# Performance work log

Hardware: AMD Instinct MI355X
Metric: run time of the kernel (lower is better)

## Reference

```python
import jax, jax.numpy as jnp
import numpy as np

EPS = 1e-6
NUM_HEADS = 16

def _rms(x, w=None):
    y = x * jax.lax.rsqrt(jnp.mean(x * x, axis=-1, keepdims=True) + EPS)
    return y if w is None else y * w

def _rope(q, k, pos):
    # q,k: [B,H,T,Dh]; half-split (rotate_half) RoPE convention, base 10000
    dh = q.shape[-1]
    half = dh // 2
    freqs = 1.0 / (10000.0 ** (jnp.arange(half, dtype=jnp.float32) / half))
    ang = pos.astype(jnp.float32)[:, None] * freqs[None, :]  # [T, half]
    cos = jnp.concatenate([jnp.cos(ang), jnp.cos(ang)], -1)  # [T, Dh]
    sin = jnp.concatenate([jnp.sin(ang), jnp.sin(ang)], -1)
    def rot(v):
        v1, v2 = jnp.split(v, 2, axis=-1)
        return jnp.concatenate([-v2, v1], -1)
    return q * cos + rot(q) * sin, k * cos + rot(k) * sin


def setup_inputs() -> dict:
    key = jax.random.key(0)
    ks = jax.random.split(key, 12)
    B, T, D, H = 2, 2048, 1024, NUM_HEADS
    Dh = D // H
    Hm = 2816  # SwiGLU hidden: multiple_of*ceil(int(2*4*D/3)/256)
    s = lambda fan_in: 1.0 / np.sqrt(fan_in)
    return {
        "x": jax.random.normal(ks[0], (B, T, D), jnp.float32),
        "c": jax.random.normal(ks[1], (B, D), jnp.float32),
        "pos": jnp.arange(T, dtype=jnp.int32),
        "adaln_w": jax.random.normal(ks[2], (D, 6 * D), jnp.float32) * s(D) * 0.1,
        "adaln_b": jax.random.normal(ks[3], (6 * D,), jnp.float32) * 0.02,
        "qkv_w": jax.random.normal(ks[4], (D, 3 * D), jnp.float32) * s(D),
        "lnq_w": jnp.ones((Dh,), jnp.float32),
        "lnk_w": jnp.ones((Dh,), jnp.float32),
        "proj_w": jax.random.normal(ks[5], (D, D), jnp.float32) * s(D),
        "proj_b": jnp.zeros((D,), jnp.float32),
        "w1_w": jax.random.normal(ks[6], (D, Hm), jnp.float32) * s(D),
        "w3_w": jax.random.normal(ks[7], (D, Hm), jnp.float32) * s(D),
        "w2_w": jax.random.normal(ks[8], (Hm, D), jnp.float32) * s(Hm),
    }


def reference(x, c, pos, adaln_w, adaln_b, qkv_w, lnq_w, lnk_w, proj_w, proj_b, w1_w, w3_w, w2_w):
    B, T, D = x.shape
    H = NUM_HEADS
    Dh = D // H

    # AdaLN: SiLU -> Linear -> chunk(6)
    mods = jax.nn.silu(c) @ adaln_w + adaln_b  # [B,6D]
    shift_msa, scale_msa, gate_msa, shift_mlp, scale_mlp, gate_mlp = jnp.split(mods, 6, axis=-1)

    # norm1 (RMSNorm, no affine) + modulate along seq dim
    x_mod = _rms(x) * (1.0 + scale_msa[:, None, :]) + shift_msa[:, None, :]

    # QKV projection (no bias)
    qkv = x_mod @ qkv_w  # [B,T,3D]
    q, k, v = jnp.split(qkv, 3, axis=-1)
    q = q.reshape(B, T, H, Dh).transpose(0, 2, 1, 3)  # [B,H,T,Dh]
    k = k.reshape(B, T, H, Dh).transpose(0, 2, 1, 3)
    v = v.reshape(B, T, H, Dh).transpose(0, 2, 1, 3)

    # per-head RMS qk-norm with affine weight
    q = _rms(q, lnq_w)
    k = _rms(k, lnk_w)

    # 1D RoPE
    q, k = _rope(q, k, pos)

    # attention core (SDPA, delegated in the original module)
    scores = jnp.einsum('bhqd,bhkd->bhqk', q, k) / jnp.sqrt(jnp.float32(Dh))
    attn = jax.nn.softmax(scores, axis=-1)
    attn_out = jnp.einsum('bhqk,bhkd->bhqd', attn, v)  # [B,H,T,Dh]
    attn_out = attn_out.transpose(0, 2, 1, 3).reshape(B, T, D)

    # post_attention: gated residual + SwiGLU MLP
    x = x + gate_msa[:, None, :] * (attn_out @ proj_w + proj_b)
    h = _rms(x) * (1.0 + scale_mlp[:, None, :]) + shift_mlp[:, None, :]
    mlp = (jax.nn.silu(h @ w1_w) * (h @ w3_w)) @ w2_w
    x = x + gate_mlp[:, None, :] * mlp
    return x
```

## Files before the change

### kernel.cpp

```cpp
#include <hip/hip_runtime.h>
#include <stdint.h>
#include <math.h>

typedef unsigned short u16;
typedef __attribute__((ext_vector_type(4))) float f32x4;
typedef __attribute__((ext_vector_type(16))) float f32x16;
typedef __attribute__((ext_vector_type(8))) __bf16 bf16x8;

#define DEV static __device__ __forceinline__

typedef __attribute__((address_space(1))) void gvoid;
typedef __attribute__((address_space(3))) void lvoid;

DEV float bf2f(u16 u){ uint32_t v = ((uint32_t)u) << 16; float f; __builtin_memcpy(&f, &v, 4); return f; }
DEV u16 f2bf(float f){ uint32_t v; __builtin_memcpy(&v, &f, 4); v = (v + 0x7fffu + ((v >> 16) & 1u)) >> 16; return (u16)v; }

DEV void cp16(const void* g, void* l){
  __builtin_amdgcn_global_load_lds((gvoid*)g, (lvoid*)l, 16, 0, 0);
}
DEV f32x4 mfma16(bf16x8 a, bf16x8 b, f32x4 c){
  return __builtin_amdgcn_mfma_f32_16x16x32_bf16(a, b, c, 0, 0, 0);
}
DEV f32x16 mfma32(bf16x8 a, bf16x8 b, f32x16 c){
  return __builtin_amdgcn_mfma_f32_32x32x16_bf16(a, b, c, 0, 0, 0);
}
DEV uint32_t cvtpk(float a, float b){
  uint32_t r;
  asm volatile("v_cvt_pk_bf16_f32 %0, %1, %2" : "=v"(r) : "v"(a), "v"(b));
  return r;
}
DEV void uswap(uint32_t& a, uint32_t& b){
  asm volatile("v_permlane32_swap_b32 %0, %1" : "+v"(a), "+v"(b));
}
DEV void fswap(float& a, float& b){
  asm volatile("v_permlane32_swap_b32 %0, %1" : "+v"(a), "+v"(b));
}
DEV float fexp2(float x){
  float r;
  asm("v_exp_f32 %0, %1" : "=v"(r) : "v"(x));
  return r;
}

DEV void slab_remap(int SX, int SY, int& bx, int& by)
{
  const int GX = gridDim.x;
  const int h = blockIdx.y * GX + blockIdx.x;
  const int x = h & 7, s = h >> 3;
  const int ssz = SX * SY;
  const int nsx = GX / SX;
  const int slab = x + 8 * (s / ssz);
  const int ws = s % ssz;
  bx = (slab % nsx) * SX + ws % SX;
  by = (slab / nsx) * SY + ws / SX;
}

__global__ void __launch_bounds__(256) adaln1(const float* __restrict__ c,
                                              const float* __restrict__ w,
                                              float* __restrict__ part)
{
  __shared__ float sc[256];
  int k0 = blockIdx.y * 128;
  {
    int i = threadIdx.x;
    int b = i >> 7, kk = i & 127;
    float v = c[b * 1024 + k0 + kk];
    sc[i] = v / (1.f + __expf(-v));
  }
  __syncthreads();
  int col = blockIdx.x * 256 + threadIdx.x;
  float a0 = 0.f, a1 = 0.f;
  #pragma unroll 8
  for (int k = 0; k < 128; ++k){
    float wv = w[(size_t)(k0 + k) * 6144 + col];
    a0 += sc[k] * wv;
    a1 += sc[128 + k] * wv;
  }
  part[((size_t)blockIdx.y * 2 + 0) * 6144 + col] = a0;
  part[((size_t)blockIdx.y * 2 + 1) * 6144 + col] = a1;
}

__global__ void __launch_bounds__(256) adaln2(const float* __restrict__ part,
                                              const float* __restrict__ bias,
                                              float* __restrict__ mods)
{
  int i = blockIdx.x * 256 + threadIdx.x;
  int b = i / 6144, col = i % 6144;
  float a = bias[col];
  #pragma unroll
  for (int r = 0; r < 8; ++r) a += part[((size_t)r * 2 + b) * 6144 + col];
  mods[i] = a;
}

__global__ void __launch_bounds__(256) rope_table(const int* __restrict__ pos,
                                                  float* __restrict__ ct,
                                                  float* __restrict__ st)
{
  int idx = blockIdx.x * 256 + threadIdx.x;
  int t = idx >> 5, i = idx & 31;
  float freq = expf(-0.28782313662425575f * (float)i);
  float ang = (float)pos[t] * freq;
  ct[idx] = cosf(ang);
  st[idx] = sinf(ang);
}

__global__ void __launch_bounds__(256) rmsmod(const float* __restrict__ x,
                                              const float* __restrict__ mods,
                                              u16* __restrict__ out,
                                              int shift_off, int scale_off)
{
  __shared__ float wsum[4];
  int row = blockIdx.x;
  int b = row >> 11;
  const float4 v = ((const float4*)(x + (size_t)row * 1024))[threadIdx.x];
  float ss = v.x * v.x + v.y * v.y + v.z * v.z + v.w * v.w;
  #pragma unroll
  for (int m = 1; m < 64; m <<= 1) ss += __shfl_xor(ss, m);
  if ((threadIdx.x & 63) == 0) wsum[threadIdx.x >> 6] = ss;
  __syncthreads();
  float tot = wsum[0] + wsum[1] + wsum[2] + wsum[3];
  float rr = rsqrtf(tot * (1.f / 1024.f) + 1e-6f);
  const float* mb = mods + (size_t)b * 6144;
  int d0 = threadIdx.x * 4;
  ushort4 o;
  o.x = f2bf(v.x * rr * (1.f + mb[scale_off + d0 + 0]) + mb[shift_off + d0 + 0]);
  o.y = f2bf(v.y * rr * (1.f + mb[scale_off + d0 + 1]) + mb[shift_off + d0 + 1]);
  o.z = f2bf(v.z * rr * (1.f + mb[scale_off + d0 + 2]) + mb[shift_off + d0 + 2]);
  o.w = f2bf(v.w * rr * (1.f + mb[scale_off + d0 + 3]) + mb[shift_off + d0 + 3]);
  ((ushort4*)(out + (size_t)row * 1024))[threadIdx.x] = o;
}

__global__ void __launch_bounds__(256) transpose_w(const float* __restrict__ in,
                                                   u16* __restrict__ out, int R, int C)
{
  __shared__ float t[32][33];
  int tx = threadIdx.x & 31, ty = threadIdx.x >> 5;
  int c0 = blockIdx.x * 32, r0 = blockIdx.y * 32;
  #pragma unroll
  for (int i = 0; i < 4; ++i) t[ty + 8 * i][tx] = in[(size_t)(r0 + ty + 8 * i) * C + c0 + tx];
  __syncthreads();
  #pragma unroll
  for (int i = 0; i < 4; ++i) out[(size_t)(c0 + ty + 8 * i) * R + r0 + tx] = f2bf(t[tx][ty + 8 * i]);
}

__global__ void __launch_bounds__(256) vtrans(const u16* __restrict__ qkv,
                                              u16* __restrict__ vt)
{
  __shared__ u16 tile[32][33];
  int tx = threadIdx.x & 31, ty = threadIdx.x >> 5;
  int t0 = blockIdx.x * 32;
  int d0 = blockIdx.y * 32;
  int bh = blockIdx.z; int b = bh >> 4, h = bh & 15;
  #pragma unroll
  for (int i = 0; i < 4; ++i) {
    int t = t0 + ty + 8 * i;
    tile[ty + 8 * i][tx] = qkv[((size_t)(b * 2048 + t)) * 3072 + 2048 + h * 64 + d0 + tx];
  }
  __syncthreads();
  #pragma unroll
  for (int i = 0; i < 4; ++i) {
    int d = d0 + ty + 8 * i;
    vt[((size_t)bh * 64 + d) * 2048 + t0 + tx] = tile[tx][ty + 8 * i];
  }
}

__global__ void __launch_bounds__(256) gemm_bt(const u16* __restrict__ A,
                                               const u16* __restrict__ Bt,
                                               int M, int N, int K,
                                               int SX, int SY,
                                               u16* __restrict__ outb)
{
  __shared__ __align__(16) u16 Ash[2][128 * 64];
  __shared__ __align__(16) u16 Bsh[2][128 * 64];
  const int tid = threadIdx.x;
  const int l = tid & 63, w = tid >> 6;
  int bx, by; slab_remap(SX, SY, bx, by);
  const int m0 = by * 128, n0 = bx * 128;
  const int wr = (w >> 1) * 64, wc = (w & 1) * 64;
  const int fr = l & 15, fg = l >> 4;
  const int sw = fr & 7;
  const int nk = K >> 6;
  f32x4 acc[4][4] = {};

  auto stage = [&](int kt, int bsel) {
    #pragma unroll
    for (int p = 0; p < 4; ++p) {
      int slot = p * 256 + tid;
      int r = slot >> 3, kp = slot & 7;
      int kpg = kp ^ (r & 7);
      cp16(A + (size_t)(m0 + r) * K + kt + kpg * 8, &Ash[bsel][slot * 8]);
      cp16(Bt + (size_t)(n0 + r) * K + kt + kpg * 8, &Bsh[bsel][slot * 8]);
    }
  };

  stage(0, 0);
  __syncthreads();

  for (int t = 0; t < nk; ++t) {
    if (t + 1 < nk) stage((t + 1) << 6, (t + 1) & 1);
    const u16* Ab = Ash[t & 1];
    const u16* Bb = Bsh[t & 1];
    #pragma unroll
    for (int kk = 0; kk < 2; ++kk) {
      const int coff = ((kk * 4 + fg) ^ sw) * 8;
      bf16x8 af[4], bfr[4];
      #pragma unroll
      for (int m = 0; m < 4; ++m) af[m] = *(const bf16x8*)(Ab + (wr + m * 16 + fr) * 64 + coff);
      #pragma unroll
      for (int n = 0; n < 4; ++n) bfr[n] = *(const bf16x8*)(Bb + (wc + n * 16 + fr) * 64 + coff);
      #pragma unroll
      for (int m = 0; m < 4; ++m)
        #pragma unroll
        for (int n = 0; n < 4; ++n)
          acc[m][n] = mfma16(af[m], bfr[n], acc[m][n]);
    }
    __syncthreads();
  }

  #pragma unroll
  for (int m = 0; m < 4; ++m)
  #pragma unroll
  for (int n = 0; n < 4; ++n)
  #pragma unroll
  for (int j = 0; j < 4; ++j) {
    int row = m0 + wr + m * 16 + fg * 4 + j;
    int col = n0 + wc + n * 16 + fr;
    outb[(size_t)row * N + col] = f2bf(acc[m][n][j]);
  }
}

template<int EPI>
__global__ void __launch_bounds__(256) gemm_skinny(const u16* __restrict__ A,
                                                   const u16* __restrict__ Bt,
                                                   int M, int N, int K,
                                                   const float* __restrict__ mods,
                                                   int gate_off,
                                                   const float* __restrict__ bias,
                                                   const float* __restrict__ res,
                                                   float* __restrict__ outf)
{
  __shared__ __align__(16) u16 Ash[2][64 * 64];
  __shared__ __align__(16) u16 Bsh[2][128 * 64];
  const int tid = threadIdx.x;
  const int l = tid & 63, w = tid >> 6;
  int bx, by; slab_remap(2, 16, bx, by);
  const int m0 = by * 64, n0 = bx * 128;
  const int wr = (w >> 1) * 32, wc = (w & 1) * 64;
  const int fr = l & 15, fg = l >> 4;
  const int sw = fr & 7;
  const int nk = K >> 6;
  f32x4 acc[2][4] = {};

  auto stage = [&](int kt, int bsel) {
    #pragma unroll
    for (int p = 0; p < 2; ++p) {
      int slot = p * 256 + tid;
      int r = slot >> 3, kp = slot & 7;
      int kpg = kp ^ (r & 7);
      cp16(A + (size_t)(m0 + r) * K + kt + kpg * 8, &Ash[bsel][slot * 8]);
    }
    #pragma unroll
    for (int p = 0; p < 4; ++p) {
      int slot = p * 256 + tid;
      int r = slot >> 3, kp = slot & 7;
      int kpg = kp ^ (r & 7);
      cp16(Bt + (size_t)(n0 + r) * K + kt + kpg * 8, &Bsh[bsel][slot * 8]);
    }
  };

  stage(0, 0);
  __syncthreads();

  for (int t = 0; t < nk; ++t) {
    if (t + 1 < nk) stage((t + 1) << 6, (t + 1) & 1);
    const u16* Ab = Ash[t & 1];
    const u16* Bb = Bsh[t & 1];
    #pragma unroll
    for (int kk = 0; kk < 2; ++kk) {
      const int coff = ((kk * 4 + fg) ^ sw) * 8;
      bf16x8 af[2], bfr[4];
      #pragma unroll
      for (int m = 0; m < 2; ++m) af[m] = *(const bf16x8*)(Ab + (wr + m * 16 + fr) * 64 + coff);
      #pragma unroll
      for (int n = 0; n < 4; ++n) bfr[n] = *(const bf16x8*)(Bb + (wc + n * 16 + fr) * 64 + coff);
      #pragma unroll
      for (int m = 0; m < 2; ++m)
        #pragma unroll
        for (int n = 0; n < 4; ++n)
          acc[m][n] = mfma16(af[m], bfr[n], acc[m][n]);
    }
    __syncthreads();
  }

  #pragma unroll
  for (int m = 0; m < 2; ++m)
  #pragma unroll
  for (int n = 0; n < 4; ++n)
  #pragma unroll
  for (int j = 0; j < 4; ++j) {
    int row = m0 + wr + m * 16 + fg * 4 + j;
    int col = n0 + wc + n * 16 + fr;
    size_t idx = (size_t)row * N + col;
    float v = acc[m][n][j];
    int b = row >> 11;
    if (EPI == 1)
      outf[idx] = res[idx] + mods[(size_t)b * 6144 + gate_off + col] * (v + bias[col]);
    else
      outf[idx] = res[idx] + mods[(size_t)b * 6144 + gate_off + col] * v;
  }
}

__global__ void __launch_bounds__(256) gemm_w13(const u16* __restrict__ A,
                                                const u16* __restrict__ B1t,
                                                const u16* __restrict__ B3t,
                                                u16* __restrict__ outb)
{
  const int K = 1024, N = 2816;
  __shared__ __align__(16) u16 Ash[2][128 * 64];
  __shared__ __align__(16) u16 B1sh[2][64 * 64];
  __shared__ __align__(16) u16 B3sh[2][64 * 64];
  const int tid = threadIdx.x;
  const int l = tid & 63, w = tid >> 6;
  int bx, by; slab_remap(11, 8, bx, by);
  const int m0 = by * 128, n0 = bx * 64;
  const int wr = (w >> 1) * 64, wc = (w & 1) * 32;
  const int fr = l & 15, fg = l >> 4;
  const int sw = fr & 7;
  f32x4 acc1[4][2] = {}, acc3[4][2] = {};

  auto stage = [&](int kt, int bsel) {
    #pragma unroll
    for (int p = 0; p < 4; ++p) {
      int slot = p * 256 + tid;
      int r = slot >> 3, kp = slot & 7;
      int kpg = kp ^ (r & 7);
      cp16(A + (size_t)(m0 + r) * K + kt + kpg * 8, &Ash[bsel][slot * 8]);
    }
    #pragma unroll
    for (int p = 0; p < 2; ++p) {
      int slot = p * 256 + tid;
      int r = slot >> 3, kp = slot & 7;
      int kpg = kp ^ (r & 7);
      cp16(B1t + (size_t)(n0 + r) * K + kt + kpg * 8, &B1sh[bsel][slot * 8]);
      cp16(B3t + (size_t)(n0 + r) * K + kt + kpg * 8, &B3sh[bsel][slot * 8]);
    }
  };

  stage(0, 0);
  __syncthreads();

  for (int t = 0; t < 16; ++t) {
    if (t + 1 < 16) stage((t + 1) << 6, (t + 1) & 1);
    const u16* Ab  = Ash[t & 1];
    const u16* B1b = B1sh[t & 1];
    const u16* B3b = B3sh[t & 1];
    #pragma unroll
    for (int kk = 0; kk < 2; ++kk) {
      const int coff = ((kk * 4 + fg) ^ sw) * 8;
      bf16x8 af[4], b1f[2], b3f[2];
      #pragma unroll
      for (int m = 0; m < 4; ++m) af[m] = *(const bf16x8*)(Ab + (wr + m * 16 + fr) * 64 + coff);
      #pragma unroll
      for (int n = 0; n < 2; ++n) {
        b1f[n] = *(const bf16x8*)(B1b + (wc + n * 16 + fr) * 64 + coff);
        b3f[n] = *(const bf16x8*)(B3b + (wc + n * 16 + fr) * 64 + coff);
      }
      #pragma unroll
      for (int m = 0; m < 4; ++m)
        #pragma unroll
        for (int n = 0; n < 2; ++n) {
          acc1[m][n] = mfma16(af[m], b1f[n], acc1[m][n]);
          acc3[m][n] = mfma16(af[m], b3f[n], acc3[m][n]);
        }
    }
    __syncthreads();
  }

  #pragma unroll
  for (int m = 0; m < 4; ++m)
  #pragma unroll
  for (int n = 0; n < 2; ++n)
  #pragma unroll
  for (int j = 0; j < 4; ++j) {
    int row = m0 + wr + m * 16 + fg * 4 + j;
    int col = n0 + wc + n * 16 + fr;
    float v1 = acc1[m][n][j];
    float v3 = acc3[m][n][j];
    float s = v1 / (1.f + __expf(-v1));
    outb[(size_t)row * N + col] = f2bf(s * v3);
  }
}

__global__ void __launch_bounds__(256) qknorm_rope(const u16* __restrict__ qkv,
                                                   const float* __restrict__ lnq,
                                                   const float* __restrict__ lnk,
                                                   const float* __restrict__ ctab,
                                                   const float* __restrict__ stab,
                                                   u16* __restrict__ qo,
                                                   u16* __restrict__ ko)
{
  int r = blockIdx.x * 4 + (threadIdx.x >> 6);
  int l = threadIdx.x & 63;
  int h = r & 15, t = (r >> 4) & 2047, b = r >> 15;
  const u16* base = qkv + ((size_t)(b * 2048 + t)) * 3072 + h * 64 + l;
  float q = bf2f(base[0]);
  float k = bf2f(base[1024]);
  float sq = q * q, sk = k * k;
  #pragma unroll
  for (int m = 1; m < 64; m <<= 1) { sq += __shfl_xor(sq, m); sk += __shfl_xor(sk, m); }
  float rq = rsqrtf(sq * (1.f / 64.f) + 1e-6f);
  float rk = rsqrtf(sk * (1.f / 64.f) + 1e-6f);
  float yq = q * rq * lnq[l];
  float yk = k * rk * lnk[l];
  float cs = ctab[t * 32 + (l & 31)];
  float sn = stab[t * 32 + (l & 31)];
  float pq = __shfl_xor(yq, 32);
  float pk = __shfl_xor(yk, 32);
  float rotq = (l < 32) ? -pq : pq;
  float rotk = (l < 32) ? -pk : pk;
  float oq = (yq * cs + rotq * sn) * 0.1803368801111204f;
  float ok = yk * cs + rotk * sn;
  size_t oidx = ((size_t)(b * 16 + h) * 2048 + t) * 64 + l;
  qo[oidx] = f2bf(oq);
  ko[oidx] = f2bf(ok);
}

__global__ void __launch_bounds__(256, 2) flash_attn(const u16* __restrict__ qg,
                                                     const u16* __restrict__ kg,
                                                     const u16* __restrict__ vtg,
                                                     u16* __restrict__ og)
{
  __shared__ __align__(16) char smem[65536];
  const int tid = threadIdx.x, l = tid & 63, w = tid >> 6;
  const int lq = l & 31, hi = l >> 5;
  const int swz = lq & 7;
  const int xcd = blockIdx.x & 7, slot = blockIdx.x >> 3;
  const int g = slot >> 4, qt = slot & 15;
  const int bh = g * 8 + xcd;
  const int h = bh & 15, b = bh >> 4;

  bf16x8 qf[4];
  {
    const u16* qp = qg + ((size_t)bh * 2048 + qt * 128 + w * 32 + lq) * 64 + hi * 8;
    #pragma unroll
    for (int ks = 0; ks < 4; ++ks) qf[ks] = *(const bf16x8*)(qp + ks * 16);
  }
  const u16* kgb = kg + (size_t)bh * 2048 * 64;
  const u16* vgb = vtg + (size_t)bh * 64 * 2048;

  auto stage = [&](int kv, int bsel) {
    #pragma unroll
    for (int p = 0; p < 4; ++p) {
      int s2 = p * 256 + tid;
      int r = s2 >> 3, cl = s2 & 7;
      int cg = cl ^ (r & 7);
      cp16(kgb + (size_t)(kv + r) * 64 + cg * 8, smem + bsel * 16384 + s2 * 16);
    }
    #pragma unroll
    for (int p = 0; p < 4; ++p) {
      int s2 = p * 256 + tid;
      int r = s2 >> 4, cl = s2 & 15;
      int cg = cl ^ (r & 7);
      cp16(vgb + (size_t)r * 2048 + kv + cg * 8, smem + 32768 + bsel * 16384 + s2 * 16);
    }
  };

  f32x16 ob0 = {}, ob1 = {};
  float l_run = 0.f;

  stage(0, 0);
  __syncthreads();

  for (int t = 0; t < 16; ++t) {
    const int cur = t & 1;
    stage(((t + 1) & 15) * 128, cur ^ 1);
    const char* Kb = smem + cur * 16384;
    const char* Vb = smem + 32768 + cur * 16384;

    #pragma unroll
    for (int ko = 0; ko < 128; ko += 64) {
      f32x16 s0 = {}, s1 = {};
      __builtin_amdgcn_s_setprio(1);
      #pragma unroll
      for (int ks = 0; ks < 4; ++ks) {
        const int c = hi + ks * 2;
        bf16x8 kf0 = *(const bf16x8*)(Kb + (ko + lq) * 128 + ((c ^ swz) << 4));
        bf16x8 kf1 = *(const bf16x8*)(Kb + (ko + 32 + lq) * 128 + ((c ^ swz) << 4));
        s0 = mfma32(kf0, qf[ks], s0);
        s1 = mfma32(kf1, qf[ks], s1);
      }
      __builtin_amdgcn_s_setprio(0);
      #pragma unroll
      for (int r = 0; r < 16; ++r) s0[r] = fexp2(s0[r]);
      #pragma unroll
      for (int r = 0; r < 16; ++r) s1[r] = fexp2(s1[r]);
      {
        float t0 = (s0[0] + s0[1]) + (s0[2] + s0[3]);
        float t1 = (s0[4] + s0[5]) + (s0[6] + s0[7]);
        float t2 = (s0[8] + s0[9]) + (s0[10] + s0[11]);
        float t3 = (s0[12] + s0[13]) + (s0[14] + s0[15]);
        float u0 = (s1[0] + s1[1]) + (s1[2] + s1[3]);
        float u1 = (s1[4] + s1[5]) + (s1[6] + s1[7]);
        float u2 = (s1[8] + s1[9]) + (s1[10] + s1[11]);
        float u3 = (s1[12] + s1[13]) + (s1[14] + s1[15]);
        float ls = ((t0 + t1) + (t2 + t3)) + ((u0 + u1) + (u2 + u3));
        float lo = ls;
        fswap(ls, lo);
        l_run += ls + lo;
      }
      uint32_t pw[16];
      {
        uint32_t x0 = cvtpk(s0[0], s0[1]),   y0 = cvtpk(s0[4], s0[5]);   uswap(x0, y0);
        uint32_t x1 = cvtpk(s0[2], s0[3]),   y1 = cvtpk(s0[6], s0[7]);   uswap(x1, y1);
        uint32_t x2 = cvtpk(s0[8], s0[9]),   y2 = cvtpk(s0[12], s0[13]); uswap(x2, y2);
        uint32_t x3 = cvtpk(s0[10], s0[11]), y3 = cvtpk(s0[14], s0[15]); uswap(x3, y3);
        pw[0] = x0; pw[1] = x1; pw[2] = y0; pw[3] = y1;
        pw[4] = x2; pw[5] = x3; pw[6] = y2; pw[7] = y3;
      }
      {
        uint32_t x0 = cvtpk(s1[0], s1[1]),   y0 = cvtpk(s1[4], s1[5]);   uswap(x0, y0);
        uint32_t x1 = cvtpk(s1[2], s1[3]),   y1 = cvtpk(s1[6], s1[7]);   uswap(x1, y1);
        uint32_t x2 = cvtpk(s1[8], s1[9]),   y2 = cvtpk(s1[12], s1[13]); uswap(x2, y2);
        uint32_t x3 = cvtpk(s1[10], s1[11]), y3 = cvtpk(s1[14], s1[15]); uswap(x3, y3);
        pw[8] = x0;  pw[9] = x1;  pw[10] = y0; pw[11] = y1;
        pw[12] = x2; pw[13] = x3; pw[14] = y2; pw[15] = y3;
      }
      __builtin_amdgcn_s_setprio(1);
      #pragma unroll
      for (int ks = 0; ks < 4; ++ks) {
        union { uint32_t u[4]; bf16x8 v; } pk_;
        pk_.u[0] = pw[ks * 4 + 0]; pk_.u[1] = pw[ks * 4 + 1];
        pk_.u[2] = pw[ks * 4 + 2]; pk_.u[3] = pw[ks * 4 + 3];
        const int c = (ko >> 3) + ks * 2 + hi;
        bf16x8 vf0 = *(const bf16x8*)(Vb + lq * 256 + ((c ^ swz) << 4));
        bf16x8 vf1 = *(const bf16x8*)(Vb + (32 + lq) * 256 + ((c ^ swz) << 4));
        ob0 = mfma32(vf0, pk_.v, ob0);
        ob1 = mfma32(vf1, pk_.v, ob1);
      }
      __builtin_amdgcn_s_setprio(0);
    }
    __syncthreads();
  }

  float invl = 1.0f / l_run;
  char* ob_base = smem + w * 4096 + lq * 128 + 8 * hi;
  #pragma unroll
  for (int g2 = 0; g2 < 4; ++g2) {
    uint2 t2;
    t2.x = cvtpk(ob0[g2 * 4 + 0] * invl, ob0[g2 * 4 + 1] * invl);
    t2.y = cvtpk(ob0[g2 * 4 + 2] * invl, ob0[g2 * 4 + 3] * invl);
    *(uint2*)(ob_base + ((g2 ^ (lq & 7)) << 4)) = t2;
    uint2 t3;
    t3.x = cvtpk(ob1[g2 * 4 + 0] * invl, ob1[g2 * 4 + 1] * invl);
    t3.y = cvtpk(ob1[g2 * 4 + 2] * invl, ob1[g2 * 4 + 3] * invl);
    *(uint2*)(ob_base + (((g2 + 4) ^ (lq & 7)) << 4)) = t3;
  }
  __syncthreads();
  #pragma unroll
  for (int i = 0; i < 4; ++i) {
    int idx = i * 256 + tid;
    int ww = idx >> 8, q = (idx >> 3) & 31, s = idx & 7;
    uint4 val = *(const uint4*)(smem + ww * 4096 + q * 128 + ((s ^ (q & 7)) << 4));
    int t = qt * 128 + ww * 32 + q;
    *(uint4*)(og + ((size_t)(b * 2048 + t)) * 1024 + h * 64 + s * 8) = val;
  }
}

extern "C" void kernel_launch(void* const* d_in, const int* in_sizes, int n_in,
                              void* d_out, int out_size, void* d_ws, size_t ws_size,
                              hipStream_t stream)
{
  (void)in_sizes; (void)n_in; (void)out_size; (void)ws_size;
  const float* x       = (const float*)d_in[0];
  const float* c       = (const float*)d_in[1];
  const int*   pos     = (const int*)d_in[2];
  const float* adaln_w = (const float*)d_in[3];
  const float* adaln_b = (const float*)d_in[4];
  const float* qkv_w   = (const float*)d_in[5];
  const float* lnq     = (const float*)d_in[6];
  const float* lnk     = (const float*)d_in[7];
  const float* proj_w  = (const float*)d_in[8];
  const float* proj_b  = (const float*)d_in[9];
  const float* w1_w    = (const float*)d_in[10];
  const float* w3_w    = (const float*)d_in[11];
  const float* w2_w    = (const float*)d_in[12];
  float* out = (float*)d_out;

  char* ws = (char*)d_ws;
  size_t off = 0;
  auto alloc = [&](size_t bytes) -> char* {
    char* p = ws + off; off += (bytes + 255) & ~(size_t)255; return p;
  };
  float* part    = (float*)alloc((size_t)8 * 2 * 6144 * 4);
  float* mods    = (float*)alloc((size_t)2 * 6144 * 4);
  float* ctab    = (float*)alloc((size_t)2048 * 32 * 4);
  float* stab    = (float*)alloc((size_t)2048 * 32 * 4);
  u16* qkv_wt    = (u16*)alloc((size_t)3072 * 1024 * 2);
  u16* proj_wt   = (u16*)alloc((size_t)1024 * 1024 * 2);
  u16* w1_wt     = (u16*)alloc((size_t)2816 * 1024 * 2);
  u16* w3_wt     = (u16*)alloc((size_t)2816 * 1024 * 2);
  u16* w2_wt     = (u16*)alloc((size_t)1024 * 2816 * 2);
  float* x1      = (float*)alloc((size_t)4096 * 1024 * 4);
  u16* attn_bf   = (u16*)alloc((size_t)4096 * 1024 * 2);
  char* pool = ws + off;
  u16* xmod_bf   = (u16*)(pool);
  u16* qkv_bf    = (u16*)(pool + 8388608);
  u16* q_bf      = (u16*)(pool + 33554432);
  u16* k_bf      = (u16*)(pool + 41943040);
  u16* vt_bf     = (u16*)(pool + 50331648);
  u16* h_bf      = (u16*)(pool);
  u16* hidden_bf = (u16*)(pool + 31457280);

  adaln1<<<dim3(24, 8), 256, 0, stream>>>(c, adaln_w, part);
  adaln2<<<48, 256, 0, stream>>>(part, adaln_b, mods);
  rope_table<<<256, 256, 0, stream>>>(pos, ctab, stab);
  rmsmod<<<4096, 256, 0, stream>>>(x, mods, xmod_bf, 0, 1024);
  transpose_w<<<dim3(96, 32), 256, 0, stream>>>(qkv_w, qkv_wt, 1024, 3072);
  transpose_w<<<dim3(32, 32), 256, 0, stream>>>(proj_w, proj_wt, 1024, 1024);
  transpose_w<<<dim3(88, 32), 256, 0, stream>>>(w1_w, w1_wt, 1024, 2816);
  transpose_w<<<dim3(88, 32), 256, 0, stream>>>(w3_w, w3_wt, 1024, 2816);
  transpose_w<<<dim3(32, 88), 256, 0, stream>>>(w2_w, w2_wt, 2816, 1024);

  gemm_bt<<<dim3(24, 32), 256, 0, stream>>>(xmod_bf, qkv_wt, 4096, 3072, 1024, 6, 8, qkv_bf);
  qknorm_rope<<<16384, 256, 0, stream>>>(qkv_bf, lnq, lnk, ctab, stab, q_bf, k_bf);
  vtrans<<<dim3(64, 2, 32), 256, 0, stream>>>(qkv_bf, vt_bf);
  flash_attn<<<512, 256, 0, stream>>>(q_bf, k_bf, vt_bf, attn_bf);
  gemm_skinny<1><<<dim3(8, 64), 256, 0, stream>>>(attn_bf, proj_wt, 4096, 1024, 1024,
                                                  mods, 2048, proj_b, x, x1);
  rmsmod<<<4096, 256, 0, stream>>>(x1, mods, h_bf, 3072, 4096);
  gemm_w13<<<dim3(44, 32), 256, 0, stream>>>(h_bf, w1_wt, w3_wt, hidden_bf);
  gemm_skinny<4><<<dim3(8, 64), 256, 0, stream>>>(hidden_bf, w2_wt, 4096, 1024, 2816,
                                                  mods, 5120, nullptr, x1, out);
}
```

Before: 270.4 us.

## Replace double-buffered K=64 staging with single-buffered K=32 tiles in QKV and W13 GEMMs

Drops the double-buffered 64-wide K staging (with an async prefetch of the next tile) from gemm_bt and gemm_w13. In its place is a single-buffered 32-wide K loop that syncs, loads, syncs and computes, with a simpler 4-way XOR swizzle. This cuts LDS usage a lot, which may allow more blocks per CU, but global-load latency is no longer overlapped with MFMA work and barriers per K element double. The slab_remap group size for w13 also changes from 8 to 4.

```diff
diff --git a/kernel.cpp b/kernel.cpp
--- a/kernel.cpp
+++ b/kernel.cpp
@@ -169,51 +169,43 @@
                                                int SX, int SY,
                                                u16* __restrict__ outb)
 {
-  __shared__ __align__(16) u16 Ash[2][128 * 64];
-  __shared__ __align__(16) u16 Bsh[2][128 * 64];
+  __shared__ __align__(16) u16 Ash[128 * 32];
+  __shared__ __align__(16) u16 Bsh[128 * 32];
   const int tid = threadIdx.x;
   const int l = tid & 63, w = tid >> 6;
   int bx, by; slab_remap(SX, SY, bx, by);
   const int m0 = by * 128, n0 = bx * 128;
   const int wr = (w >> 1) * 64, wc = (w & 1) * 64;
   const int fr = l & 15, fg = l >> 4;
-  const int sw = fr & 7;
-  const int nk = K >> 6;
   f32x4 acc[4][4] = {};
 
-  auto stage = [&](int kt, int bsel) {
-    #pragma unroll
-    for (int p = 0; p < 4; ++p) {
+  for (int kt = 0; kt < K; kt += 32) {
+    __syncthreads();
+    #pragma unroll
+    for (int p = 0; p < 2; ++p) {
       int slot = p * 256 + tid;
-      int r = slot >> 3, kp = slot & 7;
-      int kpg = kp ^ (r & 7);
-      cp16(A + (size_t)(m0 + r) * K + kt + kpg * 8, &Ash[bsel][slot * 8]);
-      cp16(Bt + (size_t)(n0 + r) * K + kt + kpg * 8, &Bsh[bsel][slot * 8]);
-    }
-  };
-
-  stage(0, 0);
-  __syncthreads();
-
-  for (int t = 0; t < nk; ++t) {
-    if (t + 1 < nk) stage((t + 1) << 6, (t + 1) & 1);
-    const u16* Ab = Ash[t & 1];
-    const u16* Bb = Bsh[t & 1];
-    #pragma unroll
-    for (int kk = 0; kk < 2; ++kk) {
-      const int coff = ((kk * 4 + fg) ^ sw) * 8;
-      bf16x8 af[4], bfr[4];
-      #pragma unroll
-      for (int m = 0; m < 4; ++m) af[m] = *(const bf16x8*)(Ab + (wr + m * 16 + fr) * 64 + coff);
-      #pragma unroll
-      for (int n = 0; n < 4; ++n) bfr[n] = *(const bf16x8*)(Bb + (wc + n * 16 + fr) * 64 + coff);
-      #pragma unroll
-      for (int m = 0; m < 4; ++m)
-        #pragma unroll
-        for (int n = 0; n < 4; ++n)
-          acc[m][n] = mfma16(af[m], bfr[n], acc[m][n]);
+      int r = slot >> 2, kp = slot & 3;
+      int kpg = kp ^ (r & 3);
+      cp16(A + (size_t)(m0 + r) * K + kt + kpg * 8, Ash + slot * 8);
+      cp16(Bt + (size_t)(n0 + r) * K + kt + kpg * 8, Bsh + slot * 8);
     }
     __syncthreads();
+    bf16x8 af[4], bfr[4];
+    #pragma unroll
+    for (int m = 0; m < 4; ++m) {
+      int r = wr + m * 16 + fr;
+      af[m] = *(const bf16x8*)(Ash + r * 32 + ((fg ^ (r & 3)) << 3));
+    }
+    #pragma unroll
+    for (int n = 0; n < 4; ++n) {
+      int r = wc + n * 16 + fr;
+      bfr[n] = *(const bf16x8*)(Bsh + r * 32 + ((fg ^ (r & 3)) << 3));
+    }
+    #pragma unroll
+    for (int m = 0; m < 4; ++m)
+      #pragma unroll
+      for (int n = 0; n < 4; ++n)
+        acc[m][n] = mfma16(af[m], bfr[n], acc[m][n]);
   }
 
   #pragma unroll
@@ -315,64 +307,53 @@
                                                 u16* __restrict__ outb)
 {
   const int K = 1024, N = 2816;
-  __shared__ __align__(16) u16 Ash[2][128 * 64];
-  __shared__ __align__(16) u16 B1sh[2][64 * 64];
-  __shared__ __align__(16) u16 B3sh[2][64 * 64];
+  __shared__ __align__(16) u16 Ash[128 * 32];
+  __shared__ __align__(16) u16 B1sh[64 * 32];
+  __shared__ __align__(16) u16 B3sh[64 * 32];
   const int tid = threadIdx.x;
   const int l = tid & 63, w = tid >> 6;
-  int bx, by; slab_remap(11, 8, bx, by);
+  int bx, by; slab_remap(11, 4, bx, by);
   const int m0 = by * 128, n0 = bx * 64;
   const int wr = (w >> 1) * 64, wc = (w & 1) * 32;
   const int fr = l & 15, fg = l >> 4;
-  const int sw = fr & 7;
   f32x4 acc1[4][2] = {}, acc3[4][2] = {};
 
-  auto stage = [&](int kt, int bsel) {
-    #pragma unroll
-    for (int p = 0; p < 4; ++p) {
-      int slot = p * 256 + tid;
-      int r = slot >> 3, kp = slot & 7;
-      int kpg = kp ^ (r & 7);
-      cp16(A + (size_t)(m0 + r) * K + kt + kpg * 8, &Ash[bsel][slot * 8]);
-    }
+  for (int kt = 0; kt < K; kt += 32) {
+    __syncthreads();
     #pragma unroll
     for (int p = 0; p < 2; ++p) {
       int slot = p * 256 + tid;
-      int r = slot >> 3, kp = slot & 7;
-      int kpg = kp ^ (r & 7);
-      cp16(B1t + (size_t)(n0 + r) * K + kt + kpg * 8, &B1sh[bsel][slot * 8]);
-      cp16(B3t + (size_t)(n0 + r) * K + kt + kpg * 8, &B3sh[bsel][slot * 8]);
-    }
-  };
-
-  stage(0, 0);
-  __syncthreads();
-
-  for (int t = 0; t < 16; ++t) {
-    if (t + 1 < 16) stage((t + 1) << 6, (t + 1) & 1);
-    const u16* Ab  = Ash[t & 1];
-    const u16* B1b = B1sh[t & 1];
-    const u16* B3b = B3sh[t & 1];
-    #pragma unroll
-    for (int kk = 0; kk < 2; ++kk) {
-      const int coff = ((kk * 4 + fg) ^ sw) * 8;
-      bf16x8 af[4], b1f[2], b3f[2];
-      #pragma unroll
-      for (int m = 0; m < 4; ++m) af[m] = *(const bf16x8*)(Ab + (wr + m * 16 + fr) * 64 + coff);
+      int r = slot >> 2, kp = slot & 3;
+      int kpg = kp ^ (r & 3);
+      cp16(A + (size_t)(m0 + r) * K + kt + kpg * 8, Ash + slot * 8);
+    }
+    {
+      int slot = tid;
+      int r = slot >> 2, kp = slot & 3;
+      int kpg = kp ^ (r & 3);
+      cp16(B1t + (size_t)(n0 + r) * K + kt + kpg * 8, B1sh + slot * 8);
+      cp16(B3t + (size_t)(n0 + r) * K + kt + kpg * 8, B3sh + slot * 8);
+    }
+    __syncthreads();
+    bf16x8 af[4], b1f[2], b3f[2];
+    #pragma unroll
+    for (int m = 0; m < 4; ++m) {
+      int r = wr + m * 16 + fr;
+      af[m] = *(const bf16x8*)(Ash + r * 32 + ((fg ^ (r & 3)) << 3));
+    }
+    #pragma unroll
+    for (int n = 0; n < 2; ++n) {
+      int r = wc + n * 16 + fr;
+      b1f[n] = *(const bf16x8*)(B1sh + r * 32 + ((fg ^ (r & 3)) << 3));
+      b3f[n] = *(const bf16x8*)(B3sh + r * 32 + ((fg ^ (r & 3)) << 3));
+    }
+    #pragma unroll
+    for (int m = 0; m < 4; ++m)
       #pragma unroll
       for (int n = 0; n < 2; ++n) {
-        b1f[n] = *(const bf16x8*)(B1b + (wc + n * 16 + fr) * 64 + coff);
-        b3f[n] = *(const bf16x8*)(B3b + (wc + n * 16 + fr) * 64 + coff);
+        acc1[m][n] = mfma16(af[m], b1f[n], acc1[m][n]);
+        acc3[m][n] = mfma16(af[m], b3f[n], acc3[m][n]);
       }
-      #pragma unroll
-      for (int m = 0; m < 4; ++m)
-        #pragma unroll
-        for (int n = 0; n < 2; ++n) {
-          acc1[m][n] = mfma16(af[m], b1f[n], acc1[m][n]);
-          acc3[m][n] = mfma16(af[m], b3f[n], acc3[m][n]);
-        }
-    }
-    __syncthreads();
   }
 
   #pragma unroll
```

Measured after the change: 257.0 us. 1.05x faster.
